# Optimization experiments

Measured on AMD Instinct MI355X. Metric: run time of the kernel, lower is better.

## Reference

```python
import jax, jax.numpy as jnp
import numpy as np

B, T, I, H = 64, 1024, 128, 256

def setup_inputs() -> dict:
    key = jax.random.key(0)
    ks = jax.random.split(key, 9)
    std = 1.0 / np.sqrt(H)
    u = lambda k, shape: jax.random.uniform(k, shape, jnp.float32, -std, std)
    return {
        "x": jax.random.normal(ks[0], (B, T, I), jnp.float32),
        # layer 0: concat dim = I + H
        "Wf1": u(ks[1], (I + H, H)), "bf1": u(ks[2], (H,)),
        "Wc1": u(ks[3], (I + H, H)), "bc1": u(ks[4], (H,)),
        # layer 1: concat dim = H + H
        "Wf2": u(ks[5], (H + H, H)), "bf2": u(ks[6], (H,)),
        "Wc2": u(ks[7], (H + H, H)), "bc2": u(ks[8], (H,)),
    }

def _mgu_layer(x_seq, Wf, bf, Wc, bc):
    # x_seq: [B, T, D] -> outputs [B, T, H], final hidden [B, H]
    h0 = jnp.zeros((x_seq.shape[0], H), x_seq.dtype)
    def step(h, x_t):
        comb = jnp.concatenate([x_t, h], axis=-1)      # [B, D+H]
        f = jax.nn.sigmoid(comb @ Wf + bf)             # forget gate
        c = jnp.tanh(comb @ Wc + bc)                   # candidate
        h_new = f * h + (1.0 - f) * c
        return h_new, h_new
    hT, ys = jax.lax.scan(step, h0, jnp.swapaxes(x_seq, 0, 1))  # ys: [T, B, H]
    return jnp.swapaxes(ys, 0, 1), hT

def reference(x, Wf1, bf1, Wc1, bc1, Wf2, bf2, Wc2, bc2):
    y1, h1 = _mgu_layer(x, Wf1, bf1, Wc1, bc1)
    y2, h2 = _mgu_layer(y1, Wf2, bf2, Wc2, bc2)
    hidden = jnp.stack([h1, h2])  # [num_layers, B, H]
    return y2, hidden
```

## Files before the change

### kernel.cpp

```cpp
#include <hip/hip_runtime.h>

typedef unsigned int uint;
typedef _Float16 f16;
typedef _Float16 f16x2 __attribute__((ext_vector_type(2)));
typedef _Float16 f16x4 __attribute__((ext_vector_type(4)));
typedef _Float16 f16x8 __attribute__((ext_vector_type(8)));
typedef float f32x4 __attribute__((ext_vector_type(4)));

#define B_ 64
#define T_ 1024
#define I_ 128
#define H_ 256

__device__ __forceinline__ float fdot2u(uint w, uint h, float acc) {
  return __builtin_amdgcn_fdot2(__builtin_bit_cast(f16x2, w),
                                __builtin_bit_cast(f16x2, h), acc, false);
}

template<int CTRL>
__device__ __forceinline__ float dpp_add(float a) {
  int m = __builtin_amdgcn_update_dpp(0, __builtin_bit_cast(int, a), CTRL, 0xf, 0xf, true);
  return a + __builtin_bit_cast(float, m);
}
template<int CTRL>
__device__ __forceinline__ float dpp_mov(float a) {
  int m = __builtin_amdgcn_update_dpp(0, __builtin_bit_cast(int, a), CTRL, 0xf, 0xf, true);
  return __builtin_bit_cast(float, m);
}

template<int KIN>
__global__ void prep_wxt(const float* __restrict__ Wf, const float* __restrict__ Wc,
                         f16* __restrict__ WxT) {
  int o = blockIdx.x * 256 + threadIdx.x;
  if (o >= 512 * KIN) return;
  int n = o / KIN, k = o % KIN;
  float v = (n < 256) ? Wf[k * H_ + n] : Wc[k * H_ + (n - 256)];
  WxT[o] = (f16)v;
}

__global__ void prep_upack(const float* __restrict__ Wf, const float* __restrict__ Wc,
                           uint* __restrict__ Up, int DIN) {
  int o = blockIdx.x * 256 + threadIdx.x;
  int i = o >> 11, tid = (o >> 2) & 511, cmp = o & 3;
  int d = 4 * i + cmp;
  int j = d >> 4, kk = d & 15;
  int w = tid >> 6, l = tid & 63, g = l >> 3, kq = l & 7;
  const float* W = (w >> 2) ? Wc : Wf;
  int col = (w & 3) * 64 + 8 * g + j;
  int k = kq * 32 + 2 * kk;
  f16x2 p = { (f16)W[(DIN + k) * H_ + col], (f16)W[(DIN + k + 1) * H_ + col] };
  Up[o] = __builtin_bit_cast(uint, p);
}

template<int KFULL, bool AF32>
__global__ __launch_bounds__(256) void gemm_xpart(const void* __restrict__ Av,
    const f16* __restrict__ Bt, const float* __restrict__ bf, const float* __restrict__ bc,
    f16* __restrict__ Xg) {
  __shared__ __align__(16) f16 As[128][72];
  __shared__ __align__(16) f16 Bs[128][72];
  const int m0 = blockIdx.x * 128, n0 = blockIdx.y * 128;
  const int tid = threadIdx.x, lane = tid & 63, wid = tid >> 6;
  const int wr = wid >> 1, wc = wid & 1;
  f32x4 zero4 = {0.f, 0.f, 0.f, 0.f};
  f32x4 acc[4][4];
  #pragma unroll
  for (int i = 0; i < 4; ++i)
    #pragma unroll
    for (int j = 0; j < 4; ++j) acc[i][j] = zero4;
  const int r2 = tid >> 1, hh = tid & 1;
  for (int kb = 0; kb < KFULL / 64; ++kb) {
    const int k0 = kb * 64;
    if (kb) __syncthreads();
    if (AF32) {
      const float* A = (const float*)Av;
      const float* src = A + (size_t)(m0 + r2) * KFULL + k0 + hh * 32;
      #pragma unroll
      for (int i = 0; i < 8; ++i) {
        float4 v = *(const float4*)(src + i * 4);
        f16x4 p = { (f16)v.x, (f16)v.y, (f16)v.z, (f16)v.w };
        *(f16x4*)&As[r2][hh * 32 + i * 4] = p;
      }
    } else {
      const f16* A = (const f16*)Av;
      const f16* src = A + (size_t)(m0 + r2) * KFULL + k0 + hh * 32;
      #pragma unroll
      for (int i = 0; i < 4; ++i)
        *(uint4*)&As[r2][hh * 32 + i * 8] = *(const uint4*)(src + i * 8);
    }
    {
      const f16* src = Bt + (size_t)(n0 + r2) * KFULL + k0 + hh * 32;
      #pragma unroll
      for (int i = 0; i < 4; ++i)
        *(uint4*)&Bs[r2][hh * 32 + i * 8] = *(const uint4*)(src + i * 8);
    }
    __syncthreads();
    #pragma unroll
    for (int kt = 0; kt < 2; ++kt) {
      f16x8 af[4], bfr[4];
      #pragma unroll
      for (int i = 0; i < 4; ++i)
        af[i] = *(const f16x8*)&As[wr * 64 + i * 16 + (lane & 15)][kt * 32 + (lane >> 4) * 8];
      #pragma unroll
      for (int j = 0; j < 4; ++j)
        bfr[j] = *(const f16x8*)&Bs[wc * 64 + j * 16 + (lane & 15)][kt * 32 + (lane >> 4) * 8];
      #pragma unroll
      for (int i = 0; i < 4; ++i)
        #pragma unroll
        for (int j = 0; j < 4; ++j)
          acc[i][j] = __builtin_amdgcn_mfma_f32_16x16x32_f16(af[i], bfr[j], acc[i][j], 0, 0, 0);
    }
  }
  const float* bias = (n0 < 256) ? bf : bc;
  #pragma unroll
  for (int j = 0; j < 4; ++j) {
    const int gn = n0 + wc * 64 + j * 16 + (lane & 15);
    const float bv = bias[gn & 255];
    #pragma unroll
    for (int i = 0; i < 4; ++i) {
      #pragma unroll
      for (int reg = 0; reg < 4; ++reg) {
        const int gm = m0 + wr * 64 + i * 16 + (lane >> 4) * 4 + reg;
        Xg[(size_t)gm * 512 + gn] = (f16)(acc[i][j][reg] + bv);
      }
    }
  }
}

__global__ __launch_bounds__(512, 2) void rec(const uint* __restrict__ Wp,
    const f16* __restrict__ Xg, float* __restrict__ yf, f16* __restrict__ yh,
    float* __restrict__ hid) {
  __shared__ __align__(16) uint h2s[160];
  __shared__ float hm[H_];
  __shared__ float carr[H_];
  const int tid = threadIdx.x, lane = tid & 63, wid = tid >> 6;
  const int wq = wid & 3, gate = wid >> 2;
  const int kq = lane & 7, r = lane & 7;
  const int b = blockIdx.x;
  const int col = wq * 64 + lane;

  uint4 wv[32];
  const uint4* Wp4 = (const uint4*)Wp;
  #pragma unroll
  for (int i = 0; i < 32; ++i) wv[i] = Wp4[i * 512 + tid];

  if (tid < 160) h2s[tid] = 0u;
  if (tid < H_) hm[tid] = 0.f;
  __syncthreads();

  const size_t xoff = ((size_t)b * T_) * 512 + gate * 256 + wq * 64 + lane;
  float xcur = (float)Xg[xoff];

  #pragma unroll 1
  for (int t = 0; t < T_; ++t) {
    const int tn = (t + 1 < T_) ? t + 1 : t;
    const f16 xnf = Xg[xoff + (size_t)tn * 512];

    float acc[8];
    #pragma unroll
    for (int j = 0; j < 8; ++j) acc[j] = 0.f;
    const uint* hb = &h2s[kq * 20];
    #pragma unroll
    for (int q = 0; q < 4; ++q) {
      uint4 hv = *(const uint4*)(hb + q * 4);
      #pragma unroll
      for (int k2 = 0; k2 < 4; ++k2) {
        const uint hp = (k2 == 0) ? hv.x : (k2 == 1) ? hv.y : (k2 == 2) ? hv.z : hv.w;
        #pragma unroll
        for (int j = 0; j < 8; ++j) {
          const uint4 w4 = wv[j * 4 + q];
          const uint wu = (k2 == 0) ? w4.x : (k2 == 1) ? w4.y : (k2 == 2) ? w4.z : w4.w;
          acc[j] = fdot2u(wu, hp, acc[j]);
        }
      }
    }
    #pragma unroll
    for (int j = 0; j < 8; ++j) {
      float a = acc[j];
      a = dpp_add<0x141>(a);
      a = dpp_add<0x1B>(a);
      a = dpp_add<0xB1>(a);
      acc[j] = a;
    }
    float s01 = (r & 1) ? acc[1] : acc[0];
    float s23 = (r & 1) ? acc[3] : acc[2];
    float s45 = (r & 1) ? acc[5] : acc[4];
    float s67 = (r & 1) ? acc[7] : acc[6];
    float s03 = (r & 2) ? s23 : s01;
    float s47 = (r & 2) ? s67 : s45;
    float pre = ((r & 4) ? s47 : s03) + xcur;

    float fv = 0.f;
    if (gate) {
      float e2 = __expf(2.f * pre);
      carr[col] = 1.f - 2.f * __builtin_amdgcn_rcpf(e2 + 1.f);
    } else {
      fv = __builtin_amdgcn_rcpf(1.f + __expf(-pre));
    }
    __syncthreads();
    if (!gate) {
      float cv = carr[col];
      float hold = hm[col];
      float hn = cv + fv * (hold - cv);
      hm[col] = hn;
      if (yf) yf[((size_t)b * T_ + t) * H_ + col] = hn;
      if (yh) yh[((size_t)b * T_ + t) * H_ + col] = (f16)hn;
      if (t == T_ - 1) hid[b * H_ + col] = hn;
      float other = dpp_mov<0xB1>(hn);
      if (!(lane & 1)) {
        f16x2 p = { (f16)hn, (f16)other };
        int jj = col >> 1;
        h2s[(jj >> 4) * 20 + (jj & 15)] = __builtin_bit_cast(uint, p);
      }
    }
    __syncthreads();
    xcur = (float)xnf;
  }
}

extern "C" void kernel_launch(void* const* d_in, const int* in_sizes, int n_in,
                              void* d_out, int out_size, void* d_ws, size_t ws_size,
                              hipStream_t stream) {
  (void)in_sizes; (void)n_in; (void)out_size; (void)ws_size;
  const float* x   = (const float*)d_in[0];
  const float* Wf1 = (const float*)d_in[1];
  const float* bf1 = (const float*)d_in[2];
  const float* Wc1 = (const float*)d_in[3];
  const float* bc1 = (const float*)d_in[4];
  const float* Wf2 = (const float*)d_in[5];
  const float* bf2 = (const float*)d_in[6];
  const float* Wc2 = (const float*)d_in[7];
  const float* bc2 = (const float*)d_in[8];
  float* out = (float*)d_out;

  char* ws = (char*)d_ws;
  f16*  Xg   = (f16*)(ws);
  f16*  y1h  = (f16*)(ws + 67108864);
  f16*  Wx1T = (f16*)(ws + 100663296);
  f16*  Wx2T = (f16*)(ws + 100794368);
  uint* Up1  = (uint*)(ws + 101056512);
  uint* Up2  = (uint*)(ws + 101318656);

  float* y2   = out;
  float* hid1 = out + (size_t)B_ * T_ * H_;
  float* hid2 = hid1 + (size_t)B_ * H_;

  prep_wxt<128><<<256, 256, 0, stream>>>(Wf1, Wc1, Wx1T);
  prep_wxt<256><<<512, 256, 0, stream>>>(Wf2, Wc2, Wx2T);
  prep_upack<<<256, 256, 0, stream>>>(Wf1, Wc1, Up1, 128);
  prep_upack<<<256, 256, 0, stream>>>(Wf2, Wc2, Up2, 256);

  gemm_xpart<128, true ><<<dim3(512, 4), 256, 0, stream>>>(x,   Wx1T, bf1, bc1, Xg);
  rec<<<64, 512, 0, stream>>>(Up1, Xg, nullptr, y1h, hid1);
  gemm_xpart<256, false><<<dim3(512, 4), 256, 0, stream>>>(y1h, Wx2T, bf2, bc2, Xg);
  rec<<<64, 512, 0, stream>>>(Up2, Xg, y2, nullptr, hid2);
}
```

Baseline: 2.010 ms.

## Batch 16 sequences per block and compute recurrence with MFMA

```diff
diff --git a/kernel.cpp b/kernel.cpp
--- a/kernel.cpp
+++ b/kernel.cpp
@@ -11,22 +11,6 @@
 #define T_ 1024
 #define I_ 128
 #define H_ 256
-
-__device__ __forceinline__ float fdot2u(uint w, uint h, float acc) {
-  return __builtin_amdgcn_fdot2(__builtin_bit_cast(f16x2, w),
-                                __builtin_bit_cast(f16x2, h), acc, false);
-}
-
-template<int CTRL>
-__device__ __forceinline__ float dpp_add(float a) {
-  int m = __builtin_amdgcn_update_dpp(0, __builtin_bit_cast(int, a), CTRL, 0xf, 0xf, true);
-  return a + __builtin_bit_cast(float, m);
-}
-template<int CTRL>
-__device__ __forceinline__ float dpp_mov(float a) {
-  int m = __builtin_amdgcn_update_dpp(0, __builtin_bit_cast(int, a), CTRL, 0xf, 0xf, true);
-  return __builtin_bit_cast(float, m);
-}
 
 template<int KIN>
 __global__ void prep_wxt(const float* __restrict__ Wf, const float* __restrict__ Wc,
@@ -38,18 +22,12 @@
   WxT[o] = (f16)v;
 }
 
-__global__ void prep_upack(const float* __restrict__ Wf, const float* __restrict__ Wc,
-                           uint* __restrict__ Up, int DIN) {
+__global__ void prep_ut(const float* __restrict__ Wf, const float* __restrict__ Wc,
+                        f16* __restrict__ UT, int DIN) {
   int o = blockIdx.x * 256 + threadIdx.x;
-  int i = o >> 11, tid = (o >> 2) & 511, cmp = o & 3;
-  int d = 4 * i + cmp;
-  int j = d >> 4, kk = d & 15;
-  int w = tid >> 6, l = tid & 63, g = l >> 3, kq = l & 7;
-  const float* W = (w >> 2) ? Wc : Wf;
-  int col = (w & 3) * 64 + 8 * g + j;
-  int k = kq * 32 + 2 * kk;
-  f16x2 p = { (f16)W[(DIN + k) * H_ + col], (f16)W[(DIN + k + 1) * H_ + col] };
-  Up[o] = __builtin_bit_cast(uint, p);
+  int n = o >> 8, k = o & 255;
+  const float* W = (n < 256) ? Wf : Wc;
+  UT[o] = (f16)W[(DIN + k) * H_ + (n & 255)];
 }
 
 template<int KFULL, bool AF32>
@@ -126,94 +104,107 @@
   }
 }
 
-__global__ __launch_bounds__(512, 2) void rec(const uint* __restrict__ Wp,
+__global__ __launch_bounds__(512, 2) void rec(const f16* __restrict__ UT,
     const f16* __restrict__ Xg, float* __restrict__ yf, f16* __restrict__ yh,
     float* __restrict__ hid) {
-  __shared__ __align__(16) uint h2s[160];
-  __shared__ float hm[H_];
-  __shared__ float carr[H_];
-  const int tid = threadIdx.x, lane = tid & 63, wid = tid >> 6;
-  const int wq = wid & 3, gate = wid >> 2;
-  const int kq = lane & 7, r = lane & 7;
-  const int b = blockIdx.x;
-  const int col = wq * 64 + lane;
-
-  uint4 wv[32];
-  const uint4* Wp4 = (const uint4*)Wp;
-  #pragma unroll
-  for (int i = 0; i < 32; ++i) wv[i] = Wp4[i * 512 + tid];
-
-  if (tid < 160) h2s[tid] = 0u;
-  if (tid < H_) hm[tid] = 0.f;
+  __shared__ __align__(16) f16 hbuf[2][16][264];
+  const int tid = threadIdx.x;
+  const int lane = tid & 63, w = tid >> 6;
+  const int lr = lane & 15, lg = lane >> 4;
+  const int m0 = blockIdx.x * 16;
+
+  int nt[4] = { 32 * w, 32 * w + 16, 256 + 32 * w, 256 + 32 * w + 16 };
+
+  f16x8 uw[4][8];
+  #pragma unroll
+  for (int tt = 0; tt < 4; ++tt)
+    #pragma unroll
+    for (int kf = 0; kf < 8; ++kf)
+      uw[tt][kf] = *(const f16x8*)&UT[(size_t)(nt[tt] + lr) * 256 + kf * 32 + lg * 8];
+
+  {
+    uint* hz = (uint*)&hbuf[0][0][0];
+    for (int i = tid; i < 2112; i += 512) hz[i] = 0u;
+  }
+
+  const f16* xp[4];
+  #pragma unroll
+  for (int tt = 0; tt < 4; ++tt)
+    xp[tt] = Xg + ((size_t)(m0 + lr) * T_) * 512 + nt[tt] + 4 * lg;
+
+  float hreg[2][4] = {{0.f,0.f,0.f,0.f},{0.f,0.f,0.f,0.f}};
+  f16x4 xcur[4];
+  #pragma unroll
+  for (int tt = 0; tt < 4; ++tt) xcur[tt] = *(const f16x4*)xp[tt];
+
+  const size_t ybase = (size_t)(m0 + lr) * T_ * H_;
+  const int ycol0 = 32 * w + 4 * lg;
+
   __syncthreads();
-
-  const size_t xoff = ((size_t)b * T_) * 512 + gate * 256 + wq * 64 + lane;
-  float xcur = (float)Xg[xoff];
 
   #pragma unroll 1
   for (int t = 0; t < T_; ++t) {
+    f16x8 hf[8];
+    #pragma unroll
+    for (int kf = 0; kf < 8; ++kf)
+      hf[kf] = *(const f16x8*)&hbuf[t & 1][lr][kf * 32 + lg * 8];
+
     const int tn = (t + 1 < T_) ? t + 1 : t;
-    const f16 xnf = Xg[xoff + (size_t)tn * 512];
-
-    float acc[8];
-    #pragma unroll
-    for (int j = 0; j < 8; ++j) acc[j] = 0.f;
-    const uint* hb = &h2s[kq * 20];
-    #pragma unroll
-    for (int q = 0; q < 4; ++q) {
-      uint4 hv = *(const uint4*)(hb + q * 4);
-      #pragma unroll
-      for (int k2 = 0; k2 < 4; ++k2) {
-        const uint hp = (k2 == 0) ? hv.x : (k2 == 1) ? hv.y : (k2 == 2) ? hv.z : hv.w;
-        #pragma unroll
-        for (int j = 0; j < 8; ++j) {
-          const uint4 w4 = wv[j * 4 + q];
-          const uint wu = (k2 == 0) ? w4.x : (k2 == 1) ? w4.y : (k2 == 2) ? w4.z : w4.w;
-          acc[j] = fdot2u(wu, hp, acc[j]);
-        }
-      }
-    }
-    #pragma unroll
-    for (int j = 0; j < 8; ++j) {
-      float a = acc[j];
-      a = dpp_add<0x141>(a);
-      a = dpp_add<0x1B>(a);
-      a = dpp_add<0xB1>(a);
-      acc[j] = a;
-    }
-    float s01 = (r & 1) ? acc[1] : acc[0];
-    float s23 = (r & 1) ? acc[3] : acc[2];
-    float s45 = (r & 1) ? acc[5] : acc[4];
-    float s67 = (r & 1) ? acc[7] : acc[6];
-    float s03 = (r & 2) ? s23 : s01;
-    float s47 = (r & 2) ? s67 : s45;
-    float pre = ((r & 4) ? s47 : s03) + xcur;
-
-    float fv = 0.f;
-    if (gate) {
-      float e2 = __expf(2.f * pre);
-      carr[col] = 1.f - 2.f * __builtin_amdgcn_rcpf(e2 + 1.f);
-    } else {
-      fv = __builtin_amdgcn_rcpf(1.f + __expf(-pre));
-    }
-    __syncthreads();
-    if (!gate) {
-      float cv = carr[col];
-      float hold = hm[col];
-      float hn = cv + fv * (hold - cv);
-      hm[col] = hn;
-      if (yf) yf[((size_t)b * T_ + t) * H_ + col] = hn;
-      if (yh) yh[((size_t)b * T_ + t) * H_ + col] = (f16)hn;
-      if (t == T_ - 1) hid[b * H_ + col] = hn;
-      float other = dpp_mov<0xB1>(hn);
-      if (!(lane & 1)) {
-        f16x2 p = { (f16)hn, (f16)other };
-        int jj = col >> 1;
-        h2s[(jj >> 4) * 20 + (jj & 15)] = __builtin_bit_cast(uint, p);
-      }
-    }
-    __syncthreads();
-    xcur = (float)xnf;
+    f16x4 xn[4];
+    #pragma unroll
+    for (int tt = 0; tt < 4; ++tt) xn[tt] = *(const f16x4*)(xp[tt] + (size_t)tn * 512);
+
+    f32x4 acc[4];
+    #pragma unroll
+    for (int tt = 0; tt < 4; ++tt) acc[tt] = (f32x4){0.f, 0.f, 0.f, 0.f};
+    #pragma unroll
+    for (int kf = 0; kf < 8; ++kf)
+      #pragma unroll
+      for (int tt = 0; tt < 4; ++tt)
+        acc[tt] = __builtin_amdgcn_mfma_f32_16x16x32_f16(uw[tt][kf], hf[kf], acc[tt], 0, 0, 0);
+
+    f16x4 hn4[2];
+    #pragma unroll
+    for (int p = 0; p < 2; ++p) {
+      #pragma unroll
+      for (int r = 0; r < 4; ++r) {
+        float pf = acc[p][r]     + (float)xcur[p][r];
+        float pc = acc[2 + p][r] + (float)xcur[2 + p][r];
+        float f  = __builtin_amdgcn_rcpf(1.f + __expf(-pf));
+        float e2 = __expf(2.f * pc);
+        float c  = 1.f - 2.f * __builtin_amdgcn_rcpf(e2 + 1.f);
+        float hn = c + f * (hreg[p][r] - c);
+        hreg[p][r] = hn;
+        hn4[p][r] = (f16)hn;
+      }
+      *(f16x4*)&hbuf[(t + 1) & 1][lr][ycol0 + 16 * p] = hn4[p];
+    }
+    if (yh) {
+      #pragma unroll
+      for (int p = 0; p < 2; ++p)
+        *(f16x4*)(yh + ybase + (size_t)t * H_ + ycol0 + 16 * p) = hn4[p];
+    }
+    if (yf) {
+      #pragma unroll
+      for (int p = 0; p < 2; ++p) {
+        float4 yv = make_float4(hreg[p][0], hreg[p][1], hreg[p][2], hreg[p][3]);
+        *(float4*)(yf + ybase + (size_t)t * H_ + ycol0 + 16 * p) = yv;
+      }
+    }
+    if (t == T_ - 1) {
+      #pragma unroll
+      for (int p = 0; p < 2; ++p) {
+        float4 hv = make_float4(hreg[p][0], hreg[p][1], hreg[p][2], hreg[p][3]);
+        *(float4*)(hid + (size_t)(m0 + lr) * H_ + ycol0 + 16 * p) = hv;
+      }
+    }
+
+    asm volatile("s_waitcnt lgkmcnt(0)" ::: "memory");
+    __builtin_amdgcn_s_barrier();
+    asm volatile("" ::: "memory");
+
+    #pragma unroll
+    for (int tt = 0; tt < 4; ++tt) xcur[tt] = xn[tt];
   }
 }
 
@@ -237,8 +228,8 @@
   f16*  y1h  = (f16*)(ws + 67108864);
   f16*  Wx1T = (f16*)(ws + 100663296);
   f16*  Wx2T = (f16*)(ws + 100794368);
-  uint* Up1  = (uint*)(ws + 101056512);
-  uint* Up2  = (uint*)(ws + 101318656);
+  f16*  UT1  = (f16*)(ws + 101056512);
+  f16*  UT2  = (f16*)(ws + 101318656);
 
   float* y2   = out;
   float* hid1 = out + (size_t)B_ * T_ * H_;
@@ -246,11 +237,11 @@
 
   prep_wxt<128><<<256, 256, 0, stream>>>(Wf1, Wc1, Wx1T);
   prep_wxt<256><<<512, 256, 0, stream>>>(Wf2, Wc2, Wx2T);
-  prep_upack<<<256, 256, 0, stream>>>(Wf1, Wc1, Up1, 128);
-  prep_upack<<<256, 256, 0, stream>>>(Wf2, Wc2, Up2, 256);
+  prep_ut<<<512, 256, 0, stream>>>(Wf1, Wc1, UT1, 128);
+  prep_ut<<<512, 256, 0, stream>>>(Wf2, Wc2, UT2, 256);
 
   gemm_xpart<128, true ><<<dim3(512, 4), 256, 0, stream>>>(x,   Wx1T, bf1, bc1, Xg);
-  rec<<<64, 512, 0, stream>>>(Up1, Xg, nullptr, y1h, hid1);
+  rec<<<4, 512, 0, stream>>>(UT1, Xg, nullptr, y1h, hid1);
   gemm_xpart<256, false><<<dim3(512, 4), 256, 0, stream>>>(y1h, Wx2T, bf2, bc2, Xg);
-  rec<<<64, 512, 0, stream>>>(Up2, Xg, y2, nullptr, hid2);
-}
+  rec<<<4, 512, 0, stream>>>(UT2, Xg, y2, nullptr, hid2);
+}
```

After: 2.625 ms. 30.6% more time.
